# Kernel tuning notes

Hardware: AMD Instinct MI355X
Metric: run time of the kernel (lower is better)

Reference implementation:

```python
import jax, jax.numpy as jnp
import numpy as np

NUM_HEADS = 32
NUM_KV_HEADS = 8
HEAD_DIM = 128
HIDDEN = 4096
B, L = 2, 4096


def _phi(x):
    # feature map: elu(x) + 1
    return jax.nn.elu(x) + 1.0


def setup_inputs() -> dict:
    key = jax.random.key(0)
    ks = jax.random.split(key, 9)
    s = 1.0 / np.sqrt(HIDDEN)
    return {
        "hidden_states": jax.random.normal(ks[0], (B, L, HIDDEN), jnp.float32),
        "Wq": jax.random.normal(ks[1], (HIDDEN, HIDDEN), jnp.float32) * s,
        "bq": jnp.zeros((HIDDEN,), jnp.float32),
        "Wk": jax.random.normal(ks[2], (NUM_KV_HEADS * HEAD_DIM, HIDDEN), jnp.float32) * s,
        "bk": jnp.zeros((NUM_KV_HEADS * HEAD_DIM,), jnp.float32),
        "Wv": jax.random.normal(ks[3], (NUM_KV_HEADS * HEAD_DIM, HIDDEN), jnp.float32) * s,
        "bv": jnp.zeros((NUM_KV_HEADS * HEAD_DIM,), jnp.float32),
        "Wo": jax.random.normal(ks[4], (HIDDEN, HIDDEN), jnp.float32) * s,
        "bo": jnp.zeros((HIDDEN,), jnp.float32),
    }


def reference(hidden_states, Wq, bq, Wk, bk, Wv, bv, Wo, bo):
    bsz, q_len, _ = hidden_states.shape
    n_rep = NUM_HEADS // NUM_KV_HEADS

    # projections (nn.Linear: y = x @ W.T + b)
    q = hidden_states @ Wq.T + bq          # [B, L, H*D]
    k = hidden_states @ Wk.T + bk          # [B, L, Hkv*D]
    v = hidden_states @ Wv.T + bv

    q = q.reshape(bsz, q_len, NUM_HEADS, HEAD_DIM).transpose(0, 2, 1, 3)       # [B,H,L,D]
    k = k.reshape(bsz, q_len, NUM_KV_HEADS, HEAD_DIM).transpose(0, 2, 1, 3)    # [B,Hkv,L,D]
    v = v.reshape(bsz, q_len, NUM_KV_HEADS, HEAD_DIM).transpose(0, 2, 1, 3)

    # repeat_kv: [B,Hkv,L,D] -> [B,H,L,D]
    k = jnp.broadcast_to(k[:, :, None], (bsz, NUM_KV_HEADS, n_rep, q_len, HEAD_DIM)).reshape(bsz, NUM_HEADS, q_len, HEAD_DIM)
    v = jnp.broadcast_to(v[:, :, None], (bsz, NUM_KV_HEADS, n_rep, q_len, HEAD_DIM)).reshape(bsz, NUM_HEADS, q_len, HEAD_DIM)

    q = _phi(q)
    k = _phi(k)

    # global KV summary: O(L*d^2) linear attention
    key_value = jnp.einsum('bhld,bhlv->bhvd', k, v)           # [B,H,D,D]
    attn = jnp.einsum('bhqd,bhvd->bhqv', q, key_value)        # [B,H,L,D]

    # normalizer: sum of feature-mapped keys over sequence, per channel
    normalizer = k.sum(axis=2)[:, :, None, :]                  # [B,H,1,D]
    attn = attn / (normalizer + 1e-10)

    attn = attn.transpose(0, 2, 1, 3).reshape(bsz, q_len, HIDDEN)
    return attn @ Wo.T + bo
```

## Files before the change

### kernel.cpp

```cpp
#include <hip/hip_runtime.h>

#define HIDDEN 4096
#define NKV 8
#define NH 32
#define HD 128
#define BATCH 2
#define SEQ 4096
#define ROWS (BATCH*SEQ)

typedef short bf16x8 __attribute__((ext_vector_type(8)));
typedef float f32x4 __attribute__((ext_vector_type(4)));

static __device__ __forceinline__ float bf2f(unsigned short u) {
    union { unsigned int i; float f; } c; c.i = ((unsigned int)u) << 16; return c.f;
}
static __device__ __forceinline__ unsigned short f2bf(float x) {
    union { float f; unsigned int i; } c; c.f = x;
    unsigned int r = c.i + 0x7fffu + ((c.i >> 16) & 1u);
    return (unsigned short)(r >> 16);
}

static __device__ __forceinline__ void gl2lds16(const void* g, void* l) {
    __builtin_amdgcn_global_load_lds(
        (const __attribute__((address_space(1))) unsigned int*)g,
        (__attribute__((address_space(3))) unsigned int*)l, 16, 0, 0);
}

#define WGBAR() __builtin_amdgcn_s_barrier()
#define VMW(n) asm volatile("s_waitcnt vmcnt(" #n ")" ::: "memory")
#define LGKM(n) asm volatile("s_waitcnt lgkmcnt(" #n ")" ::: "memory")
#define SCHED_FENCE() __builtin_amdgcn_sched_barrier(0)

__global__ __launch_bounds__(256)
void cast_kernel(const float* __restrict__ in, unsigned short* __restrict__ out, int n4) {
    int idx = blockIdx.x * blockDim.x + threadIdx.x;
    int stride = gridDim.x * blockDim.x;
    for (int i = idx; i < n4; i += stride) {
        float4 f = ((const float4*)in)[i];
        ushort4 o;
        o.x = f2bf(f.x); o.y = f2bf(f.y); o.z = f2bf(f.z); o.w = f2bf(f.w);
        ((ushort4*)out)[i] = o;
    }
}

template<int MODE>
__global__ __launch_bounds__(512, 2)
void gemm256(const unsigned short* __restrict__ A, int lda,
             const unsigned short* __restrict__ B, int ldb,
             const float* __restrict__ bias0, const float* __restrict__ bias1,
             void* __restrict__ Cout, int M, int N, int K)
{
    __shared__ __align__(16) unsigned char sm[131072];

    const int tid = threadIdx.x;
    const int wid = tid >> 6, lane = tid & 63;
    const int wr = wid >> 2, wc = wid & 3;
    const int lr = lane & 15, kg = lane >> 4;
    const int lswz = (lane & 7) << 4;

    int nbx = N >> 8;
    int nwg = nbx * (M >> 8);
    int cpx = nwg >> 3;
    int bid = (int)blockIdx.x;
    int wg = (bid & 7) * cpx + (bid >> 3);
    int bx = wg % nbx, by = wg / nbx;
    int rowBase = by << 8, colBase = bx << 8;

    size_t sA[2][2], sB[2][2];
#pragma unroll
    for (int h = 0; h < 2; ++h)
#pragma unroll
        for (int i = 0; i < 2; ++i) {
            int o = i * 8192 + wid * 1024 + lane * 16;
            int row = o >> 7;
            int ce = ((o & 127) ^ ((row & 7) << 4)) >> 1;
            sA[h][i] = (size_t)(rowBase + h * 128 + row) * lda + ce;
            sB[h][i] = (size_t)(colBase + h * 128 + row) * ldb + ce;
        }
    const int ldsW = wid * 1024;

    auto SA = [&](int nb, int h, int i, size_t ko) {
        gl2lds16(A + sA[h][i] + ko, sm + nb + h * 16384 + i * 8192 + ldsW);
    };
    auto SB = [&](int nb, int h, int i, size_t ko) {
        gl2lds16(B + sB[h][i] + ko, sm + nb + 32768 + h * 16384 + i * 8192 + ldsW);
    };

    const int aRd = wr * 16384 + (lr << 7);
    const int bRd = 32768 + (wc >> 1) * 16384 + (((wc & 1) * 64 + lr) << 7);
    const int kcol0 = (kg * 16) ^ lswz;
    const int kcol1 = (64 + kg * 16) ^ lswz;

    auto RA = [&](int cb, int mp, int ks) -> bf16x8 {
        return *(const bf16x8*)(sm + cb + aRd + mp * 2048 + (ks ? kcol1 : kcol0));
    };
    auto RB = [&](int cb, int n, int ks) -> bf16x8 {
        return *(const bf16x8*)(sm + cb + bRd + n * 2048 + (ks ? kcol1 : kcol0));
    };

    f32x4 acc[8][4] = {};
    bf16x8 bfr[4][2];

    auto MF = [&](bf16x8 a0, bf16x8 a1, bf16x8 a2, bf16x8 a3, int m0, int m1) {
        SCHED_FENCE();
        __builtin_amdgcn_s_setprio(1);
#pragma unroll
        for (int n = 0; n < 4; ++n) {
            acc[m0][n] = __builtin_amdgcn_mfma_f32_16x16x32_bf16(a0, bfr[n][0], acc[m0][n], 0, 0, 0);
            acc[m0][n] = __builtin_amdgcn_mfma_f32_16x16x32_bf16(a1, bfr[n][1], acc[m0][n], 0, 0, 0);
            acc[m1][n] = __builtin_amdgcn_mfma_f32_16x16x32_bf16(a2, bfr[n][0], acc[m1][n], 0, 0, 0);
            acc[m1][n] = __builtin_amdgcn_mfma_f32_16x16x32_bf16(a3, bfr[n][1], acc[m1][n], 0, 0, 0);
        }
        __builtin_amdgcn_s_setprio(0);
        SCHED_FENCE();
    };

    SCHED_FENCE();
    SB(0, 0, 0, 0); SB(0, 0, 1, 0); SB(0, 1, 0, 0); SB(0, 1, 1, 0);
    SA(0, 0, 0, 0); SA(0, 1, 0, 0); SA(0, 0, 1, 0); SA(0, 1, 1, 0);
    SCHED_FENCE();
    VMW(0);
    WGBAR();
    SCHED_FENCE();

    int cur = 0;
    size_t ko = 64;
    const int NT = K >> 6;

    for (int t = 0; t < NT - 1; ++t) {
        const int cb = cur << 16, nb = (cur ^ 1) << 16;
        SCHED_FENCE();
        SB(nb, 0, 0, ko); SB(nb, 0, 1, ko); SB(nb, 1, 0, ko); SB(nb, 1, 1, ko);
        SA(nb, 0, 0, ko); SA(nb, 1, 0, ko); SA(nb, 0, 1, ko); SA(nb, 1, 1, ko);
        SCHED_FENCE();
        bf16x8 a0 = RA(cb, 0, 0), a1 = RA(cb, 0, 1), a2 = RA(cb, 1, 0), a3 = RA(cb, 1, 1);
#pragma unroll
        for (int n = 0; n < 4; ++n) { bfr[n][0] = RB(cb, n, 0); bfr[n][1] = RB(cb, n, 1); }
        SCHED_FENCE();
        bf16x8 b0 = RA(cb, 2, 0), b1 = RA(cb, 2, 1), b2 = RA(cb, 3, 0), b3 = RA(cb, 3, 1);
        SCHED_FENCE();
        LGKM(4);
        MF(a0, a1, a2, a3, 0, 1);
        a0 = RA(cb, 4, 0); a1 = RA(cb, 4, 1); a2 = RA(cb, 5, 0); a3 = RA(cb, 5, 1);
        SCHED_FENCE();
        LGKM(4);
        MF(b0, b1, b2, b3, 2, 3);
        b0 = RA(cb, 6, 0); b1 = RA(cb, 6, 1); b2 = RA(cb, 7, 0); b3 = RA(cb, 7, 1);
        SCHED_FENCE();
        LGKM(4);
        MF(a0, a1, a2, a3, 4, 5);
        LGKM(0);
        MF(b0, b1, b2, b3, 6, 7);
        VMW(0);
        WGBAR();
        SCHED_FENCE();
        cur ^= 1; ko += 64;
    }
    {
        const int cb = cur << 16;
        bf16x8 a0 = RA(cb, 0, 0), a1 = RA(cb, 0, 1), a2 = RA(cb, 1, 0), a3 = RA(cb, 1, 1);
#pragma unroll
        for (int n = 0; n < 4; ++n) { bfr[n][0] = RB(cb, n, 0); bfr[n][1] = RB(cb, n, 1); }
        SCHED_FENCE();
        bf16x8 b0 = RA(cb, 2, 0), b1 = RA(cb, 2, 1), b2 = RA(cb, 3, 0), b3 = RA(cb, 3, 1);
        SCHED_FENCE();
        LGKM(4);
        MF(a0, a1, a2, a3, 0, 1);
        a0 = RA(cb, 4, 0); a1 = RA(cb, 4, 1); a2 = RA(cb, 5, 0); a3 = RA(cb, 5, 1);
        SCHED_FENCE();
        LGKM(4);
        MF(b0, b1, b2, b3, 2, 3);
        b0 = RA(cb, 6, 0); b1 = RA(cb, 6, 1); b2 = RA(cb, 7, 0); b3 = RA(cb, 7, 1);
        SCHED_FENCE();
        LGKM(4);
        MF(a0, a1, a2, a3, 4, 5);
        LGKM(0);
        MF(b0, b1, b2, b3, 6, 7);
    }

    int r0 = rowBase + wr * 128 + kg * 4;
    int c0 = colBase + wc * 64 + lr;
#pragma unroll
    for (int n = 0; n < 4; ++n) {
        int col = c0 + n * 16;
        float bv;
        if (MODE == 2) bv = (col < 1024) ? bias0[col] : bias1[col - 1024];
        else           bv = bias0[col];
#pragma unroll
        for (int m = 0; m < 8; ++m) {
            int row = r0 + m * 16;
#pragma unroll
            for (int r = 0; r < 4; ++r) {
                float v = acc[m][n][r] + bv;
                if (MODE == 1) v = (v > 0.f) ? v + 1.f : __expf(v);
                if (MODE == 2 && col < 1024) v = (v > 0.f) ? v + 1.f : __expf(v);
                if (MODE == 0) ((float*)Cout)[(size_t)(row + r) * N + col] = v;
                else ((unsigned short*)Cout)[(size_t)(row + r) * N + col] = f2bf(v);
            }
        }
    }
}

__global__ __launch_bounds__(256)
void kv_partial(const unsigned short* __restrict__ Kb, const unsigned short* __restrict__ Vb,
                int ld, float* __restrict__ kvp, float* __restrict__ ksp)
{
    int chunk = blockIdx.x;
    int g = blockIdx.y;
    int b = g >> 3, hkv = g & 7;
    __shared__ float kl[32][128];
    __shared__ float vl[32][128];
    int tid = threadIdx.x;
    int c0 = (tid >> 4) * 8, d0 = (tid & 15) * 8;
    float acc[8][8] = {};
    float ksacc = 0.0f;
    size_t rowBase = (size_t)b * SEQ + (size_t)chunk * 128;

    for (int sch = 0; sch < 4; ++sch) {
        __syncthreads();
        for (int t = tid; t < 512; t += 256) {
            int l = t >> 4, col = (t & 15) * 8;
            size_t off = (rowBase + sch * 32 + l) * ld + hkv * HD + col;
            uint4 kr = *(const uint4*)(Kb + off);
            uint4 vr = *(const uint4*)(Vb + off);
            unsigned int ku[4] = {kr.x, kr.y, kr.z, kr.w};
            unsigned int vu[4] = {vr.x, vr.y, vr.z, vr.w};
#pragma unroll
            for (int q = 0; q < 4; ++q) {
                kl[l][col + q * 2]     = bf2f((unsigned short)(ku[q] & 0xffff));
                kl[l][col + q * 2 + 1] = bf2f((unsigned short)(ku[q] >> 16));
                vl[l][col + q * 2]     = bf2f((unsigned short)(vu[q] & 0xffff));
                vl[l][col + q * 2 + 1] = bf2f((unsigned short)(vu[q] >> 16));
            }
        }
        __syncthreads();
        for (int l = 0; l < 32; ++l) {
            float vv[8], kk[8];
#pragma unroll
            for (int x = 0; x < 8; ++x) { vv[x] = vl[l][c0 + x]; kk[x] = kl[l][d0 + x]; }
#pragma unroll
            for (int x = 0; x < 8; ++x)
#pragma unroll
                for (int y = 0; y < 8; ++y)
                    acc[x][y] += vv[x] * kk[y];
        }
        if (tid < 128) {
            for (int l = 0; l < 32; ++l) ksacc += kl[l][tid];
        }
    }
    float* out = kvp + ((size_t)g * 32 + chunk) * (HD * HD);
#pragma unroll
    for (int x = 0; x < 8; ++x)
#pragma unroll
        for (int y = 0; y < 8; ++y)
            out[(c0 + x) * HD + d0 + y] = acc[x][y];
    if (tid < 128) ksp[((size_t)g * 32 + chunk) * HD + tid] = ksacc;
}

__global__ __launch_bounds__(256)
void kv_reduce(const float* __restrict__ kvp, const float* __restrict__ ksp,
               unsigned short* __restrict__ kvb, float* __restrict__ ksum)
{
    int slice = blockIdx.x;
    int g = blockIdx.y;
    int tid = threadIdx.x;
    int e = slice * 1024 + tid * 4;
    float4 s = {0.f, 0.f, 0.f, 0.f};
    for (int ch = 0; ch < 32; ++ch) {
        float4 p = *(const float4*)(kvp + ((size_t)g * 32 + ch) * (HD * HD) + e);
        s.x += p.x; s.y += p.y; s.z += p.z; s.w += p.w;
    }
    ushort4 o;
    o.x = f2bf(s.x); o.y = f2bf(s.y); o.z = f2bf(s.z); o.w = f2bf(s.w);
    *(ushort4*)(kvb + (size_t)g * HD * HD + e) = o;
    if (slice == 0 && tid < 128) {
        float ss = 0.f;
        for (int ch = 0; ch < 32; ++ch) ss += ksp[((size_t)g * 32 + ch) * HD + tid];
        ksum[g * HD + tid] = ss;
    }
}

__global__ __launch_bounds__(256)
void attn_gemm(const unsigned short* __restrict__ Q,
               const unsigned short* __restrict__ KV,
               const float* __restrict__ KS,
               unsigned short* __restrict__ Out)
{
    const int BK = 32;
    __shared__ unsigned short As[128 * BK];
    __shared__ unsigned short Bs[128 * BK];

    int rt = blockIdx.x;
    int h  = blockIdx.y;
    int g = (rt >> 5) * NKV + (h >> 2);
    int rowBase = rt << 7;

    const unsigned short* A = Q + (size_t)h * HD;
    const unsigned short* B = KV + (size_t)g * HD * HD;
    const float* ks = KS + g * HD;

    int tid = threadIdx.x;
    int wave = tid >> 6, lane = tid & 63;
    int wr = wave >> 1, wc = wave & 1;

    f32x4 acc[4][4] = {};

    int sr = lane >> 2;
    int sc = (lane & 3) * 8;

    const unsigned short* Aw = A + (size_t)(rowBase + wave * 32 + sr) * HIDDEN + sc;
    const unsigned short* Bw = B + (size_t)(wave * 32 + sr) * HD + sc;
    unsigned short* Asw = As + wave * 32 * BK;
    unsigned short* Bsw = Bs + wave * 32 * BK;

    int arow = (wr * 64 + (lane & 15)) * BK + (lane >> 4) * 8;
    int brow = (wc * 64 + (lane & 15)) * BK + (lane >> 4) * 8;

    for (int kt = 0; kt < HD; kt += BK) {
        gl2lds16(Aw + kt, Asw);
        gl2lds16(Aw + kt + (size_t)16 * HIDDEN, Asw + 16 * BK);
        gl2lds16(Bw + kt, Bsw);
        gl2lds16(Bw + kt + (size_t)16 * HD, Bsw + 16 * BK);
        __syncthreads();
        bf16x8 af[4], bfr[4];
#pragma unroll
        for (int i = 0; i < 4; ++i) af[i] = *(const bf16x8*)&As[arow + i * 16 * BK];
#pragma unroll
        for (int j = 0; j < 4; ++j) bfr[j] = *(const bf16x8*)&Bs[brow + j * 16 * BK];
#pragma unroll
        for (int i = 0; i < 4; ++i)
#pragma unroll
            for (int j = 0; j < 4; ++j)
                acc[i][j] = __builtin_amdgcn_mfma_f32_16x16x32_bf16(af[i], bfr[j], acc[i][j], 0, 0, 0);
        __syncthreads();
    }

    int r0 = rowBase + wr * 64 + ((lane >> 4) << 2);
    int c0 = wc * 64 + (lane & 15);
#pragma unroll
    for (int j = 0; j < 4; ++j) {
        int col = c0 + j * 16;
        float inv = 1.0f / (ks[col] + 1e-10f);
#pragma unroll
        for (int i = 0; i < 4; ++i) {
            int row = r0 + i * 16;
#pragma unroll
            for (int r = 0; r < 4; ++r) {
                float v = acc[i][j][r] * inv;
                Out[(size_t)(row + r) * HIDDEN + h * HD + col] = f2bf(v);
            }
        }
    }
}

extern "C" void kernel_launch(void* const* d_in, const int* in_sizes, int n_in,
                              void* d_out, int out_size, void* d_ws, size_t ws_size,
                              hipStream_t stream)
{
    const float* hs = (const float*)d_in[0];
    const float* Wq = (const float*)d_in[1];
    const float* bq = (const float*)d_in[2];
    const float* Wk = (const float*)d_in[3];
    const float* bk = (const float*)d_in[4];
    const float* Wv = (const float*)d_in[5];
    const float* bv = (const float*)d_in[6];
    const float* Wo = (const float*)d_in[7];
    const float* bo = (const float*)d_in[8];

    char* ws = (char*)d_ws;
    size_t off = 0;
    auto alloc = [&](size_t bytes) -> char* {
        char* p = ws + off;
        off += (bytes + 255) & ~(size_t)255;
        return p;
    };

    unsigned short* hs_b  = (unsigned short*)alloc((size_t)ROWS * HIDDEN * 2);
    unsigned short* Wq_b  = (unsigned short*)alloc((size_t)HIDDEN * HIDDEN * 2);
    unsigned short* Wkv_b = (unsigned short*)alloc((size_t)2048 * HIDDEN * 2);
    unsigned short* Wo_b  = (unsigned short*)alloc((size_t)HIDDEN * HIDDEN * 2);
    unsigned short* kvout = (unsigned short*)alloc((size_t)ROWS * 2048 * 2);
    float* ksp   = (float*)alloc((size_t)16 * 32 * HD * 4);
    unsigned short* kvb = (unsigned short*)alloc((size_t)16 * HD * HD * 2);
    float* ksum  = (float*)alloc((size_t)16 * HD * 4);

    float* kvp = (float*)Wq_b;
    unsigned short* attn_b = hs_b;
    unsigned short* q_b = (unsigned short*)d_out;

    (void)in_sizes; (void)n_in; (void)out_size; (void)ws_size;

    auto cast = [&](const float* in, unsigned short* out, size_t n) {
        int n4 = (int)(n / 4);
        int blocks = (n4 + 255) / 256;
        if (blocks > 2048) blocks = 2048;
        cast_kernel<<<dim3(blocks), dim3(256), 0, stream>>>(in, out, n4);
    };

    cast(hs, hs_b, (size_t)ROWS * HIDDEN);
    cast(Wq, Wq_b, (size_t)HIDDEN * HIDDEN);
    cast(Wk, Wkv_b, (size_t)1024 * HIDDEN);
    cast(Wv, Wkv_b + (size_t)1024 * HIDDEN, (size_t)1024 * HIDDEN);
    cast(Wo, Wo_b, (size_t)HIDDEN * HIDDEN);

    gemm256<1><<<dim3(512), dim3(512), 0, stream>>>(hs_b, HIDDEN, Wq_b, HIDDEN, bq, nullptr, q_b, ROWS, HIDDEN, HIDDEN);
    gemm256<2><<<dim3(256), dim3(512), 0, stream>>>(hs_b, HIDDEN, Wkv_b, HIDDEN, bk, bv, kvout, ROWS, 2048, HIDDEN);

    kv_partial<<<dim3(32, 16), dim3(256), 0, stream>>>(kvout, kvout + 1024, 2048, kvp, ksp);
    kv_reduce<<<dim3(16, 16), dim3(256), 0, stream>>>(kvp, ksp, kvb, ksum);

    attn_gemm<<<dim3(64, 32), dim3(256), 0, stream>>>(q_b, kvb, ksum, attn_b);

    gemm256<0><<<dim3(512), dim3(512), 0, stream>>>(attn_b, HIDDEN, Wo_b, HIDDEN, bo, nullptr, d_out, ROWS, HIDDEN, HIDDEN);
}
```

Measured before the change: 774.3 us.

## Switch GEMM mainloop to 4-stage K=32 LDS ring with deeper prefetch

Restructures the 256x256 GEMM mainloop from a double-buffered K=64 tile scheme to a four-slot ring of K=32 tiles, each 32KB, keeping two stages of global-to-LDS loads in flight (waiting with vmcnt(4) instead of 0). It also changes the LDS layout and swizzle so each tile packs both 128-row halves into 64-byte rows. The aim is to hide global-load latency behind MFMA work. The cost is twice as many workgroup barriers per K, and each barrier interval holds less compute.

```diff
diff --git a/kernel.cpp b/kernel.cpp
--- a/kernel.cpp
+++ b/kernel.cpp
@@ -56,7 +56,7 @@
     const int wid = tid >> 6, lane = tid & 63;
     const int wr = wid >> 2, wc = wid & 3;
     const int lr = lane & 15, kg = lane >> 4;
-    const int lswz = (lane & 7) << 4;
+    const int swz = (lane & 7) << 4;
 
     int nbx = N >> 8;
     int nwg = nbx * (M >> 8);
@@ -66,116 +66,107 @@
     int bx = wg % nbx, by = wg / nbx;
     int rowBase = by << 8, colBase = bx << 8;
 
-    size_t sA[2][2], sB[2][2];
-#pragma unroll
-    for (int h = 0; h < 2; ++h)
-#pragma unroll
-        for (int i = 0; i < 2; ++i) {
-            int o = i * 8192 + wid * 1024 + lane * 16;
-            int row = o >> 7;
-            int ce = ((o & 127) ^ ((row & 7) << 4)) >> 1;
-            sA[h][i] = (size_t)(rowBase + h * 128 + row) * lda + ce;
-            sB[h][i] = (size_t)(colBase + h * 128 + row) * ldb + ce;
-        }
+    size_t sA[2], sB[2];
+#pragma unroll
+    for (int i = 0; i < 2; ++i) {
+        int o = i * 8192 + tid * 16;
+        int rm = o >> 7;
+        int inner = (o & 127) ^ ((rm & 7) << 4);
+        int half = inner >> 6;
+        int ke = (inner & 63) >> 1;
+        sA[i] = (size_t)(rowBase + half * 128 + rm) * lda + ke;
+        sB[i] = (size_t)(colBase + half * 128 + rm) * ldb + ke;
+    }
     const int ldsW = wid * 1024;
 
-    auto SA = [&](int nb, int h, int i, size_t ko) {
-        gl2lds16(A + sA[h][i] + ko, sm + nb + h * 16384 + i * 8192 + ldsW);
-    };
-    auto SB = [&](int nb, int h, int i, size_t ko) {
-        gl2lds16(B + sB[h][i] + ko, sm + nb + 32768 + h * 16384 + i * 8192 + ldsW);
-    };
-
-    const int aRd = wr * 16384 + (lr << 7);
-    const int bRd = 32768 + (wc >> 1) * 16384 + (((wc & 1) * 64 + lr) << 7);
-    const int kcol0 = (kg * 16) ^ lswz;
-    const int kcol1 = (64 + kg * 16) ^ lswz;
-
-    auto RA = [&](int cb, int mp, int ks) -> bf16x8 {
-        return *(const bf16x8*)(sm + cb + aRd + mp * 2048 + (ks ? kcol1 : kcol0));
-    };
-    auto RB = [&](int cb, int n, int ks) -> bf16x8 {
-        return *(const bf16x8*)(sm + cb + bRd + n * 2048 + (ks ? kcol1 : kcol0));
+    auto STAGE = [&](int nb, size_t ko) {
+        gl2lds16(A + sA[0] + ko, sm + nb + 0 * 8192 + ldsW);
+        gl2lds16(A + sA[1] + ko, sm + nb + 1 * 8192 + ldsW);
+        gl2lds16(B + sB[0] + ko, sm + nb + 16384 + 0 * 8192 + ldsW);
+        gl2lds16(B + sB[1] + ko, sm + nb + 16384 + 1 * 8192 + ldsW);
+    };
+
+    const int aRd = (lr << 7) + ((((wr << 6) | (kg << 4))) ^ swz);
+    const int bRd = 16384 + ((((wc & 1) * 64 + lr)) << 7)
+                  + (((((wc >> 1) << 6) | (kg << 4))) ^ swz);
+
+    auto RA = [&](int cb, int mp) -> bf16x8 {
+        return *(const bf16x8*)(sm + cb + aRd + mp * 2048);
+    };
+    auto RB = [&](int cb, int n) -> bf16x8 {
+        return *(const bf16x8*)(sm + cb + bRd + n * 2048);
     };
 
     f32x4 acc[8][4] = {};
-    bf16x8 bfr[4][2];
-
-    auto MF = [&](bf16x8 a0, bf16x8 a1, bf16x8 a2, bf16x8 a3, int m0, int m1) {
+    bf16x8 bfr[4];
+
+    auto MF2 = [&](bf16x8 x0, bf16x8 x1, int m0, int m1) {
         SCHED_FENCE();
         __builtin_amdgcn_s_setprio(1);
 #pragma unroll
         for (int n = 0; n < 4; ++n) {
-            acc[m0][n] = __builtin_amdgcn_mfma_f32_16x16x32_bf16(a0, bfr[n][0], acc[m0][n], 0, 0, 0);
-            acc[m0][n] = __builtin_amdgcn_mfma_f32_16x16x32_bf16(a1, bfr[n][1], acc[m0][n], 0, 0, 0);
-            acc[m1][n] = __builtin_amdgcn_mfma_f32_16x16x32_bf16(a2, bfr[n][0], acc[m1][n], 0, 0, 0);
-            acc[m1][n] = __builtin_amdgcn_mfma_f32_16x16x32_bf16(a3, bfr[n][1], acc[m1][n], 0, 0, 0);
+            acc[m0][n] = __builtin_amdgcn_mfma_f32_16x16x32_bf16(x0, bfr[n], acc[m0][n], 0, 0, 0);
+            acc[m1][n] = __builtin_amdgcn_mfma_f32_16x16x32_bf16(x1, bfr[n], acc[m1][n], 0, 0, 0);
         }
         __builtin_amdgcn_s_setprio(0);
         SCHED_FENCE();
     };
 
+    auto TILE = [&](int cb) {
+        bfr[0] = RB(cb, 0); bfr[1] = RB(cb, 1); bfr[2] = RB(cb, 2); bfr[3] = RB(cb, 3);
+        bf16x8 a0 = RA(cb, 0), a1 = RA(cb, 1);
+        SCHED_FENCE();
+        bf16x8 a2 = RA(cb, 2), a3 = RA(cb, 3);
+        SCHED_FENCE();
+        LGKM(2);
+        MF2(a0, a1, 0, 1);
+        a0 = RA(cb, 4); a1 = RA(cb, 5);
+        SCHED_FENCE();
+        LGKM(2);
+        MF2(a2, a3, 2, 3);
+        a2 = RA(cb, 6); a3 = RA(cb, 7);
+        SCHED_FENCE();
+        LGKM(2);
+        MF2(a0, a1, 4, 5);
+        LGKM(0);
+        MF2(a2, a3, 6, 7);
+    };
+
+    const int NT = K >> 5;
+
     SCHED_FENCE();
-    SB(0, 0, 0, 0); SB(0, 0, 1, 0); SB(0, 1, 0, 0); SB(0, 1, 1, 0);
-    SA(0, 0, 0, 0); SA(0, 1, 0, 0); SA(0, 0, 1, 0); SA(0, 1, 1, 0);
+    STAGE(0, 0);
+    STAGE(32768, 32);
     SCHED_FENCE();
-    VMW(0);
+    VMW(4);
     WGBAR();
     SCHED_FENCE();
 
     int cur = 0;
     size_t ko = 64;
-    const int NT = K >> 6;
-
-    for (int t = 0; t < NT - 1; ++t) {
-        const int cb = cur << 16, nb = (cur ^ 1) << 16;
-        SCHED_FENCE();
-        SB(nb, 0, 0, ko); SB(nb, 0, 1, ko); SB(nb, 1, 0, ko); SB(nb, 1, 1, ko);
-        SA(nb, 0, 0, ko); SA(nb, 1, 0, ko); SA(nb, 0, 1, ko); SA(nb, 1, 1, ko);
-        SCHED_FENCE();
-        bf16x8 a0 = RA(cb, 0, 0), a1 = RA(cb, 0, 1), a2 = RA(cb, 1, 0), a3 = RA(cb, 1, 1);
-#pragma unroll
-        for (int n = 0; n < 4; ++n) { bfr[n][0] = RB(cb, n, 0); bfr[n][1] = RB(cb, n, 1); }
-        SCHED_FENCE();
-        bf16x8 b0 = RA(cb, 2, 0), b1 = RA(cb, 2, 1), b2 = RA(cb, 3, 0), b3 = RA(cb, 3, 1);
-        SCHED_FENCE();
-        LGKM(4);
-        MF(a0, a1, a2, a3, 0, 1);
-        a0 = RA(cb, 4, 0); a1 = RA(cb, 4, 1); a2 = RA(cb, 5, 0); a3 = RA(cb, 5, 1);
-        SCHED_FENCE();
-        LGKM(4);
-        MF(b0, b1, b2, b3, 2, 3);
-        b0 = RA(cb, 6, 0); b1 = RA(cb, 6, 1); b2 = RA(cb, 7, 0); b3 = RA(cb, 7, 1);
-        SCHED_FENCE();
-        LGKM(4);
-        MF(a0, a1, a2, a3, 4, 5);
-        LGKM(0);
-        MF(b0, b1, b2, b3, 6, 7);
+    for (int t = 0; t < NT - 2; ++t) {
+        const int cb = cur << 15;
+        const int nb = ((cur + 2) & 3) << 15;
+        SCHED_FENCE();
+        STAGE(nb, ko);
+        SCHED_FENCE();
+        TILE(cb);
+        VMW(4);
+        WGBAR();
+        SCHED_FENCE();
+        cur = (cur + 1) & 3; ko += 32;
+    }
+    {
+        const int cb = cur << 15;
+        TILE(cb);
         VMW(0);
         WGBAR();
         SCHED_FENCE();
-        cur ^= 1; ko += 64;
+        cur = (cur + 1) & 3;
     }
     {
-        const int cb = cur << 16;
-        bf16x8 a0 = RA(cb, 0, 0), a1 = RA(cb, 0, 1), a2 = RA(cb, 1, 0), a3 = RA(cb, 1, 1);
-#pragma unroll
-        for (int n = 0; n < 4; ++n) { bfr[n][0] = RB(cb, n, 0); bfr[n][1] = RB(cb, n, 1); }
-        SCHED_FENCE();
-        bf16x8 b0 = RA(cb, 2, 0), b1 = RA(cb, 2, 1), b2 = RA(cb, 3, 0), b3 = RA(cb, 3, 1);
-        SCHED_FENCE();
-        LGKM(4);
-        MF(a0, a1, a2, a3, 0, 1);
-        a0 = RA(cb, 4, 0); a1 = RA(cb, 4, 1); a2 = RA(cb, 5, 0); a3 = RA(cb, 5, 1);
-        SCHED_FENCE();
-        LGKM(4);
-        MF(b0, b1, b2, b3, 2, 3);
-        b0 = RA(cb, 6, 0); b1 = RA(cb, 6, 1); b2 = RA(cb, 7, 0); b3 = RA(cb, 7, 1);
-        SCHED_FENCE();
-        LGKM(4);
-        MF(a0, a1, a2, a3, 4, 5);
-        LGKM(0);
-        MF(b0, b1, b2, b3, 6, 7);
+        const int cb = cur << 15;
+        TILE(cb);
     }
 
     int r0 = rowBase + wr * 128 + kg * 4;
```

After: 796.7 us. 2.9% more time.
